# Performance work log

Measured on AMD Instinct MI355X. Metric: run time of the kernel, lower is better.

## Reference

```python
import jax, jax.numpy as jnp
import numpy as np


def _conv2d_valid(x, w):
    # x: (N, C, H, W), w: (O, C, kH, kW) -> (N, O, H-kH+1, W-kW+1)
    return jax.lax.conv_general_dilated(
        x, w, window_strides=(1, 1), padding='VALID',
        dimension_numbers=('NCHW', 'OIHW', 'NCHW'))


def setup_inputs() -> dict:
    key = jax.random.key(0)
    kx, ky = jax.random.split(key)
    x = jax.random.normal(kx, (16, 64, 128, 128), dtype=jnp.float32)
    y = jax.random.normal(ky, (64, 64, 16, 16), dtype=jnp.float32)
    return {"x": x, "y": y}


def reference(x, y):
    # Normalize each of the K kernels to unit L2 norm (sum over C, kH, kW).
    normed_y = y / jnp.sqrt(jnp.sum(y * y, axis=(1, 2, 3), keepdims=True))
    # Per-window L2 norm of x via ones-kernel box conv over x^2.
    ones_kernel = jnp.ones(y.shape, dtype=x.dtype)
    x_norm = jnp.sqrt(_conv2d_valid(x * x, ones_kernel))
    # Normalized cross-correlation, clamped at zero.
    diss = _conv2d_valid(x, normed_y) / x_norm
    return jax.nn.relu(diss)
```

## Files before the change

### kernel.cpp

```cpp
#include <hip/hip_runtime.h>
#include <stdint.h>

#define GAS __attribute__((address_space(1)))
#define LAS __attribute__((address_space(3)))

typedef __attribute__((ext_vector_type(8))) short short8;
typedef __attribute__((ext_vector_type(4))) float float4v;
typedef __attribute__((ext_vector_type(4))) unsigned int uint4v;

__device__ __forceinline__ unsigned short f2bf(float f) {
  union { float f; unsigned int u; } v; v.f = f;
  unsigned int r = v.u + 0x7fffu + ((v.u >> 16) & 1u);
  return (unsigned short)(r >> 16);
}

__device__ __forceinline__ void async_g2l16(const void* g, void* l) {
  __builtin_amdgcn_global_load_lds((const GAS unsigned int*)g,
                                   (LAS unsigned int*)l, 16, 0, 0);
}

__device__ __forceinline__ void vmem_drain() {
  asm volatile("s_waitcnt vmcnt(0)" ::: "memory");
}

__global__ void knorm_y(const float* __restrict__ y, unsigned short* __restrict__ y_t2) {
  int o = blockIdx.x;
  int tid = threadIdx.x;
  const float* yo = y + o * 16384;
  float s = 0.f;
  for (int idx = tid; idx < 16384; idx += 256) { float v = yo[idx]; s += v * v; }
  for (int off = 32; off; off >>= 1) s += __shfl_down(s, off, 64);
  __shared__ float red[4];
  if ((tid & 63) == 0) red[tid >> 6] = s;
  __syncthreads();
  float rn = 1.0f / sqrtf(red[0] + red[1] + red[2] + red[3]);
  int og = o >> 4, ol = o & 15;
  for (int idx = tid; idx < 16384; idx += 256) {
    int c = idx >> 8, dy = (idx >> 4) & 15, dx = idx & 15;
    int t = dy * 16 + dx;
    int cb = c >> 5, q = (c >> 3) & 3, j = c & 7;
    size_t dst = (size_t)t * 4096 + (size_t)(og * 2 + cb) * 512 + (q * 16 + ol) * 8 + j;
    y_t2[dst] = f2bf(yo[idx] * rn);
  }
}

__global__ void ktrans_x(const float* __restrict__ x, unsigned short* __restrict__ x_t,
                         float* __restrict__ s) {
  int h = blockIdx.x, n = blockIdx.y;
  int tid = threadIdx.x;
  __shared__ __align__(16) unsigned short tb[8192];
  __shared__ float sb[256];
  const float* xb = x + ((size_t)n * 64) * 16384 + h * 128;
  int w = tid & 127, half = tid >> 7;
  float acc = 0.f;
#pragma unroll
  for (int cs = 0; cs < 4; ++cs) {
    short8 tmp;
#pragma unroll
    for (int j = 0; j < 8; ++j) {
      int c = half * 32 + cs * 8 + j;
      float v = xb[(size_t)c * 16384 + w];
      tmp[j] = (short)f2bf(v);
      acc += v * v;
    }
    int chunk = (half * 4 + cs) ^ (w & 7);
    *(short8*)(tb + w * 64 + chunk * 8) = tmp;
  }
  sb[tid] = acc;
  __syncthreads();
  uint4v* dst = (uint4v*)(x_t + ((size_t)(n * 128 + h)) * 8192);
  const uint4v* src = (const uint4v*)tb;
  for (int idx = tid; idx < 1024; idx += 256) dst[idx] = src[idx];
  if (tid < 128) s[((size_t)(n * 128 + h)) * 128 + tid] = sb[tid] + sb[tid + 128];
}

__global__ void knorm_x(const float* __restrict__ s, float* __restrict__ invn) {
  int i = blockIdx.x, n = blockIdx.y;
  int tid = threadIdx.x;
  __shared__ float colsum[128];
  const float* sp = s + ((size_t)(n * 128 + i)) * 128;
  float a = 0.f;
#pragma unroll
  for (int dy = 0; dy < 16; ++dy) a += sp[dy * 128 + tid];
  colsum[tid] = a;
  __syncthreads();
  if (tid < 113) {
    float acc = 0.f;
#pragma unroll
    for (int dx = 0; dx < 16; ++dx) acc += colsum[tid + dx];
    invn[((size_t)n * 113 + i) * 113 + tid] = 1.0f / sqrtf(acc);
  }
}

__launch_bounds__(128, 2)
__global__ void kconv(const unsigned short* __restrict__ x_t,
                      const unsigned short* __restrict__ y_t2,
                      const float* __restrict__ invn,
                      float* __restrict__ out) {
  int i = blockIdx.x;
  int n = blockIdx.y;
  int tid = threadIdx.x;
  int lane = tid & 63, wave = tid >> 6;
  int lane15 = lane & 15, q = lane >> 4;

  __shared__ __align__(16) char smem[32768];
  char* const A0 = smem;
  char* const A1 = smem + 16384;

  const char* xrow0 = (const char*)(x_t + ((size_t)(n * 128 + i)) * 8192);

  auto stageA = [&](int dy, char* buf) {
    const char* src = xrow0 + (size_t)dy * 16384;
#pragma unroll
    for (int it = 0; it < 8; ++it) {
      int chunk = it * 128 + wave * 64;
      async_g2l16(src + (chunk + lane) * 16, buf + chunk * 16);
    }
  };

  const short8* ybase = (const short8*)y_t2 + lane;
  auto loadB = [&](int t, short8 bf[4][2]) {
    const short8* p = ybase + (size_t)t * 512;
#pragma unroll
    for (int nt = 0; nt < 4; ++nt) {
      bf[nt][0] = p[nt * 128];
      bf[nt][1] = p[nt * 128 + 64];
    }
  };

  float4v acc[4][4];
#pragma unroll
  for (int mt = 0; mt < 4; ++mt)
#pragma unroll
    for (int nt = 0; nt < 4; ++nt) acc[mt][nt] = (float4v){0.f, 0.f, 0.f, 0.f};

  int abase[4];
#pragma unroll
  for (int mt = 0; mt < 4; ++mt) abase[mt] = (wave * 64 + mt * 16 + lane15) * 128;

  short8 b0[4][2], b1[4][2];
  stageA(0, A0);
  loadB(0, b0);
  vmem_drain();
  __syncthreads();

#pragma unroll 1
  for (int dy = 0; dy < 16; ++dy) {
    char* Ab = (dy & 1) ? A1 : A0;
    if (dy < 15) {
      __builtin_amdgcn_sched_barrier(0);
      stageA(dy + 1, (dy & 1) ? A0 : A1);
      __builtin_amdgcn_sched_barrier(0);
    }
#pragma unroll
    for (int dx = 0; dx < 16; ++dx) {
      int t = dy * 16 + dx;
      short8(&bc)[4][2] = (dx & 1) ? b1 : b0;
      short8(&bn)[4][2] = (dx & 1) ? b0 : b1;
      if (t < 255) loadB(t + 1, bn);
      int xr = (lane15 + dx) & 7;
#pragma unroll
      for (int cb = 0; cb < 2; ++cb) {
        int aoff = dx * 128 + (((q + cb * 4) ^ xr) << 4);
#pragma unroll
        for (int mt = 0; mt < 4; ++mt) {
          short8 a = *(const short8*)(Ab + abase[mt] + aoff);
#pragma unroll
          for (int nt = 0; nt < 4; ++nt)
            acc[mt][nt] = __builtin_amdgcn_mfma_f32_16x16x32_bf16(a, bc[nt][cb], acc[mt][nt], 0, 0, 0);
        }
      }
    }
    asm volatile("s_waitcnt vmcnt(8)" ::: "memory");
    __syncthreads();
  }

  const float* ivp = invn + ((size_t)n * 113 + i) * 113;
  float* op = out + (size_t)n * 64 * 12769 + (size_t)i * 113;
  int jbase = wave * 64 + q * 4;
#pragma unroll
  for (int mt = 0; mt < 4; ++mt) {
    int j0 = jbase + mt * 16;
    if (j0 <= 108) {
      float4v iv = *(const float4v*)(ivp + j0);
#pragma unroll
      for (int nt = 0; nt < 4; ++nt) {
        int o = nt * 16 + lane15;
        float4v v = acc[mt][nt];
        float4v r;
        r[0] = fmaxf(v[0] * iv[0], 0.f);
        r[1] = fmaxf(v[1] * iv[1], 0.f);
        r[2] = fmaxf(v[2] * iv[2], 0.f);
        r[3] = fmaxf(v[3] * iv[3], 0.f);
        *(float4v*)(op + (size_t)o * 12769 + j0) = r;
      }
    } else if (j0 == 112) {
      float ivs = ivp[112];
#pragma unroll
      for (int nt = 0; nt < 4; ++nt) {
        int o = nt * 16 + lane15;
        op[(size_t)o * 12769 + 112] = fmaxf(acc[mt][nt][0] * ivs, 0.f);
      }
    }
  }
}

extern "C" void kernel_launch(void* const* d_in, const int* in_sizes, int n_in,
                              void* d_out, int out_size, void* d_ws, size_t ws_size,
                              hipStream_t stream) {
  const float* x = (const float*)d_in[0];
  const float* y = (const float*)d_in[1];
  float* out = (float*)d_out;
  char* ws = (char*)d_ws;
  unsigned short* x_t = (unsigned short*)ws;
  unsigned short* y_t2 = (unsigned short*)(ws + 33554432);
  float* s = (float*)(ws + 35651584);
  float* invn = (float*)(ws + 36700160);

  hipLaunchKernelGGL(knorm_y, dim3(64), dim3(256), 0, stream, y, y_t2);
  hipLaunchKernelGGL(ktrans_x, dim3(128, 16), dim3(256), 0, stream, x, x_t, s);
  hipLaunchKernelGGL(knorm_x, dim3(113, 16), dim3(128), 0, stream, s, invn);
  hipLaunchKernelGGL(kconv, dim3(113, 16), dim3(128), 0, stream, x_t, y_t2, invn, out);
}
```

Measured before the change: 561.9 us.

## Process two batch images per block to share weight loads, drop A double-buffering

Each block of the conv kernel now has four waves and covers the same output row for two batch images. The waves share each B (weight) fragment load across both images, halving weight traffic per output. The double-buffered async staging of A is replaced by a single buffer refilled between dy steps with a full drain and two barriers, which serialises load and compute. Launch bounds move to 256 threads with 3 blocks per SM, and the grid is flattened so consecutive blocks map to different image pairs.

Measured after the change: 600.4 us. 6.9% more time.

```diff
diff --git a/kernel.cpp b/kernel.cpp
--- a/kernel.cpp
+++ b/kernel.cpp
@@ -92,29 +92,32 @@
   }
 }
 
-__launch_bounds__(128, 2)
+__launch_bounds__(256, 3)
 __global__ void kconv(const unsigned short* __restrict__ x_t,
                       const unsigned short* __restrict__ y_t2,
                       const float* __restrict__ invn,
                       float* __restrict__ out) {
-  int i = blockIdx.x;
-  int n = blockIdx.y;
+  int lin = blockIdx.y * 113 + blockIdx.x;
+  int npair = lin & 7;
+  int i = lin >> 3;
+  int n0 = npair * 2;
   int tid = threadIdx.x;
   int lane = tid & 63, wave = tid >> 6;
   int lane15 = lane & 15, q = lane >> 4;
-
-  __shared__ __align__(16) char smem[32768];
-  char* const A0 = smem;
-  char* const A1 = smem + 16384;
-
-  const char* xrow0 = (const char*)(x_t + ((size_t)(n * 128 + i)) * 8192);
-
-  auto stageA = [&](int dy, char* buf) {
-    const char* src = xrow0 + (size_t)dy * 16384;
-#pragma unroll
-    for (int it = 0; it < 8; ++it) {
-      int chunk = it * 128 + wave * 64;
-      async_g2l16(src + (chunk + lane) * 16, buf + chunk * 16);
+  int nn = wave >> 1;
+  int jh = wave & 1;
+
+  __shared__ __align__(16) char smem[34816];
+
+  auto stageA2 = [&](int dy) {
+#pragma unroll
+    for (int r = 0; r < 2; ++r) {
+      const char* src = (const char*)(x_t + ((size_t)((n0 + r) * 128 + i + dy)) * 8192);
+#pragma unroll
+      for (int it = 0; it < 4; ++it) {
+        int chunk = it * 256 + wave * 64;
+        async_g2l16(src + (chunk + lane) * 16, smem + r * 16384 + chunk * 16);
+      }
     }
   };
 
@@ -136,22 +139,17 @@
 
   int abase[4];
 #pragma unroll
-  for (int mt = 0; mt < 4; ++mt) abase[mt] = (wave * 64 + mt * 16 + lane15) * 128;
+  for (int mt = 0; mt < 4; ++mt)
+    abase[mt] = nn * 16384 + (jh * 64 + mt * 16 + lane15) * 128;
 
   short8 b0[4][2], b1[4][2];
-  stageA(0, A0);
+  stageA2(0);
   loadB(0, b0);
   vmem_drain();
   __syncthreads();
 
 #pragma unroll 1
   for (int dy = 0; dy < 16; ++dy) {
-    char* Ab = (dy & 1) ? A1 : A0;
-    if (dy < 15) {
-      __builtin_amdgcn_sched_barrier(0);
-      stageA(dy + 1, (dy & 1) ? A0 : A1);
-      __builtin_amdgcn_sched_barrier(0);
-    }
 #pragma unroll
     for (int dx = 0; dx < 16; ++dx) {
       int t = dy * 16 + dx;
@@ -164,20 +162,25 @@
         int aoff = dx * 128 + (((q + cb * 4) ^ xr) << 4);
 #pragma unroll
         for (int mt = 0; mt < 4; ++mt) {
-          short8 a = *(const short8*)(Ab + abase[mt] + aoff);
+          short8 a = *(const short8*)(smem + abase[mt] + aoff);
 #pragma unroll
           for (int nt = 0; nt < 4; ++nt)
             acc[mt][nt] = __builtin_amdgcn_mfma_f32_16x16x32_bf16(a, bc[nt][cb], acc[mt][nt], 0, 0, 0);
         }
       }
     }
-    asm volatile("s_waitcnt vmcnt(8)" ::: "memory");
-    __syncthreads();
-  }
-
+    if (dy < 15) {
+      __syncthreads();
+      stageA2(dy + 1);
+      vmem_drain();
+      __syncthreads();
+    }
+  }
+
+  int n = n0 + nn;
   const float* ivp = invn + ((size_t)n * 113 + i) * 113;
   float* op = out + (size_t)n * 64 * 12769 + (size_t)i * 113;
-  int jbase = wave * 64 + q * 4;
+  int jbase = jh * 64 + q * 4;
 #pragma unroll
   for (int mt = 0; mt < 4; ++mt) {
     int j0 = jbase + mt * 16;
@@ -220,5 +223,5 @@
   hipLaunchKernelGGL(knorm_y, dim3(64), dim3(256), 0, stream, y, y_t2);
   hipLaunchKernelGGL(ktrans_x, dim3(128, 16), dim3(256), 0, stream, x, x_t, s);
   hipLaunchKernelGGL(knorm_x, dim3(113, 16), dim3(128), 0, stream, s, invn);
-  hipLaunchKernelGGL(kconv, dim3(113, 16), dim3(128), 0, stream, x_t, y_t2, invn, out);
-}
+  hipLaunchKernelGGL(kconv, dim3(113, 8), dim3(256), 0, stream, x_t, y_t2, invn, out);
+}
```
